# Kernel optimization log

Hardware: AMD Instinct MI355X
Metric: run time of the kernel (lower is better)

The kernel has to match this reference:

```python
import jax, jax.numpy as jnp
import numpy as np

HIDDEN = 4096
NUM_HEADS = 32
NUM_KV_HEADS = 8
HEAD_DIM = 128
ROPE_THETA = 10000.0


def setup_inputs() -> dict:
    key = jax.random.key(0)
    ks = jax.random.split(key, 5)
    B, N = 2, 2048
    s = 0.02
    return {
        "hidden_states": jax.random.normal(ks[0], (B, N, HIDDEN), dtype=jnp.float32),
        "positions": jnp.tile(jnp.arange(N, dtype=jnp.int32)[None, :], (B, 1)),
        "Wq": jax.random.normal(ks[1], (HIDDEN, NUM_HEADS * HEAD_DIM), dtype=jnp.float32) * s,
        "Wk": jax.random.normal(ks[2], (HIDDEN, NUM_KV_HEADS * HEAD_DIM), dtype=jnp.float32) * s,
        "Wv": jax.random.normal(ks[3], (HIDDEN, NUM_KV_HEADS * HEAD_DIM), dtype=jnp.float32) * s,
        "Wo": jax.random.normal(ks[4], (NUM_HEADS * HEAD_DIM, HIDDEN), dtype=jnp.float32) * s,
    }


def _rotate_half(x):
    half = x.shape[-1] // 2
    return jnp.concatenate([-x[..., half:], x[..., :half]], axis=-1)


def reference(hidden_states, positions, Wq, Wk, Wv, Wo):
    B, N, _ = hidden_states.shape
    H, KVH, D = NUM_HEADS, NUM_KV_HEADS, HEAD_DIM
    rep = H // KVH

    # projections
    q = (hidden_states @ Wq).reshape(B, N, H, D).transpose(0, 2, 1, 3)     # [B,H,N,D]
    k = (hidden_states @ Wk).reshape(B, N, KVH, D).transpose(0, 2, 1, 3)   # [B,KVH,N,D]
    v = (hidden_states @ Wv).reshape(B, N, KVH, D).transpose(0, 2, 1, 3)   # [B,KVH,N,D]

    # rotary embedding
    inv_freq = 1.0 / (ROPE_THETA ** (jnp.arange(0, D, 2, dtype=jnp.float32) / D))
    freqs = positions.astype(jnp.float32)[..., None] * inv_freq            # [B,N,D/2]
    emb = jnp.concatenate([freqs, freqs], axis=-1)                          # [B,N,D]
    cos = jnp.cos(emb)[:, None, :, :]                                       # [B,1,N,D]
    sin = jnp.sin(emb)[:, None, :, :]
    q = q * cos + _rotate_half(q) * sin
    k = k * cos + _rotate_half(k) * sin

    # GQA attention without materializing repeated k/v:
    # group q heads by kv head (repeat_interleave => q head h uses kv group h//rep)
    qg = q.reshape(B, KVH, rep, N, D)
    scale = 1.0 / jnp.sqrt(jnp.asarray(D, dtype=q.dtype))
    scores = jnp.einsum('bgrnd,bgmd->bgrnm', qg, k) * scale                 # [B,KVH,rep,N,N]
    causal = jnp.tril(jnp.ones((N, N), dtype=bool))
    scores = jnp.where(causal, scores, jnp.finfo(scores.dtype).min)
    attn = jax.nn.softmax(scores, axis=-1)
    out = jnp.einsum('bgrnm,bgmd->bgrnd', attn, v)                          # [B,KVH,rep,N,D]
    out = out.reshape(B, H, N, D).transpose(0, 2, 1, 3).reshape(B, N, H * D)
    return out @ Wo
```

## Files before the change

kernel.cpp:

```cpp
#include <hip/hip_runtime.h>
#include <hip/hip_bf16.h>

typedef __bf16 bf16_t;
typedef float  f32x4  __attribute__((ext_vector_type(4)));
typedef bf16_t bf16x4 __attribute__((ext_vector_type(4)));
typedef bf16_t bf16x8 __attribute__((ext_vector_type(8)));

#define MFMA16(a, b, c) __builtin_amdgcn_mfma_f32_16x16x32_bf16((a), (b), (c), 0, 0, 0)

#define GLOAD_LDS16(g, l)                                                              \
  __builtin_amdgcn_global_load_lds((const __attribute__((address_space(1))) void*)(g), \
                                   (__attribute__((address_space(3))) void*)(l), 16, 0, 0)

#define BARRIER    __builtin_amdgcn_s_barrier()
#define WAIT_LGKM0 asm volatile("s_waitcnt lgkmcnt(0)" ::: "memory")
#define WAIT_LGKM8 asm volatile("s_waitcnt lgkmcnt(8)" ::: "memory")
#define WAIT_VM3   asm volatile("s_waitcnt vmcnt(3)" ::: "memory")
#define WAIT_VM4   asm volatile("s_waitcnt vmcnt(4)" ::: "memory")
#define WAIT_VM0   asm volatile("s_waitcnt vmcnt(0)" ::: "memory")

__global__ __launch_bounds__(256) void cvt_bf16(const float* __restrict__ in,
                                                bf16_t* __restrict__ out, int n4) {
  int stride = gridDim.x * blockDim.x;
  for (int i = blockIdx.x * blockDim.x + threadIdx.x; i < n4; i += stride) {
    f32x4 v = ((const f32x4*)in)[i];
    bf16x4 o;
#pragma unroll
    for (int j = 0; j < 4; ++j) o[j] = (bf16_t)v[j];
    ((bf16x4*)out)[i] = o;
  }
}

__global__ __launch_bounds__(256) void transpose_cvt(const float* __restrict__ in,
                                                     bf16_t* __restrict__ out,
                                                     int R, int C) {
  __shared__ float t[64][65];
  int tr0 = blockIdx.y * 64, tc0 = blockIdx.x * 64;
  int tx = threadIdx.x & 15, ty = threadIdx.x >> 4;
#pragma unroll
  for (int i = 0; i < 4; ++i) {
    f32x4 v = *(const f32x4*)(in + (size_t)(tr0 + ty + 16 * i) * C + tc0 + tx * 4);
#pragma unroll
    for (int j = 0; j < 4; ++j) t[ty + 16 * i][tx * 4 + j] = v[j];
  }
  __syncthreads();
#pragma unroll
  for (int i = 0; i < 4; ++i) {
    bf16x4 o4;
#pragma unroll
    for (int j = 0; j < 4; ++j) o4[j] = (bf16_t)t[tx * 4 + j][ty + 16 * i];
    *(bf16x4*)(out + (size_t)(tc0 + ty + 16 * i) * R + tr0 + tx * 4) = o4;
  }
}

#define LDB8(bf)                                                                         \
  {                                                                                      \
    const int sb_ = bBase0 + (bf)*16384;                                                 \
    _Pragma("unroll") for (int nf = 0; nf < 4; ++nf) {                                   \
      int row_ = brow0 + nf * 16 + ci;                                                   \
      _Pragma("unroll") for (int ks = 0; ks < 2; ++ks)                                   \
          b[nf][ks] = *(const bf16x8*)&lds[sb_ + row_ * 64 + ((ks * 32 + g * 8) ^ co)];  \
    }                                                                                    \
  }

#define LDA4(bf, q)                                                                      \
  {                                                                                      \
    const int sb_ = aBase0 + (bf)*16384;                                                 \
    _Pragma("unroll") for (int j = 0; j < 2; ++j) {                                      \
      int row_ = ((q)*2 + j) * 16 + ci;                                                  \
      _Pragma("unroll") for (int ks = 0; ks < 2; ++ks)                                   \
          a[j][ks] = *(const bf16x8*)&lds[sb_ + row_ * 64 + ((ks * 32 + g * 8) ^ co)];   \
    }                                                                                    \
  }

#define MMQ(q)                                                                           \
  {                                                                                      \
    __builtin_amdgcn_s_setprio(1);                                                       \
    _Pragma("unroll") for (int j = 0; j < 2; ++j)                                        \
        _Pragma("unroll") for (int nf = 0; nf < 4; ++nf)                                 \
            _Pragma("unroll") for (int ks = 0; ks < 2; ++ks)                             \
                acc[(q)*2 + j][nf] = MFMA16(a[j][ks], b[nf][ks], acc[(q)*2 + j][nf]);    \
    __builtin_amdgcn_s_setprio(0);                                                       \
  }

template <int WRITE_BF16>
__global__ __launch_bounds__(512) void gemm8o(const bf16_t* __restrict__ A,
                                              const bf16_t* __restrict__ Bt,
                                              void* __restrict__ Cv,
                                              int N, int K, int ntn) {
  __shared__ alignas(16) bf16_t lds[65536];
  const int tid = threadIdx.x;
  const int lane = tid & 63, w = tid >> 6;
  const int wr = w >> 2, wc = w & 3;
  const int g = lane >> 4, ci = lane & 15;
  const int cpx = gridDim.x >> 3;
  const int wg = ((int)blockIdx.x & 7) * cpx + ((int)blockIdx.x >> 3);
  const int m0 = (wg / ntn) * 256, n0 = (wg % ntn) * 256;
  const int ksw = ((lane & 7) ^ (lane >> 3)) << 3;
  const int aBase0 = wr * 8192;
  const int bBase0 = 32768 + (wc >> 1) * 8192;
  const int brow0 = (wc & 1) * 64;
  const int co = (ci & 7) << 3;

  const bf16_t* As[2] = {A + (size_t)m0 * K, A + (size_t)(m0 + 128) * K};
  const bf16_t* Bs[2] = {Bt + (size_t)n0 * K, Bt + (size_t)(n0 + 128) * K};

  auto stage = [&](const bf16_t* src, int kk, int ldsbase) {
#pragma unroll
    for (int j = 0; j < 2; ++j)
      GLOAD_LDS16(src + (size_t)(j * 64 + w * 8 + (lane >> 3)) * K + kk + ksw,
                  (char*)&lds[ldsbase + (j * 64 + w * 8) * 64]);
  };

  bf16x8 a[2][2], b[4][2];
  f32x4 acc[8][4];
#pragma unroll
  for (int mf = 0; mf < 8; ++mf)
#pragma unroll
    for (int nf = 0; nf < 4; ++nf) acc[mf][nf] = f32x4{0.f, 0.f, 0.f, 0.f};

  stage(As[0], 0, 0);
  stage(As[1], 0, 8192);
  stage(Bs[0], 0, 32768);
  stage(Bs[1], 0, 40960);
  stage(Bs[0], 64, 49152);
  stage(Bs[1], 64, 57344);
  WAIT_VM4;
  BARRIER;

  const int NT2 = K >> 7;
  for (int i = 0; i < NT2; ++i) {
    const int keb = i << 7;
    const int kA1 = keb + 64;
    int e2 = keb + 128;
    if (e2 > K - 64) e2 = K - 64;
    int o2 = keb + 192;
    if (o2 > K - 64) o2 = K - 64;
    LDA4(0, 0) LDB8(0)
    stage(As[0], kA1, 16384);
    WAIT_LGKM8;
    BARRIER; WAIT_LGKM0;
    MMQ(0)
    BARRIER;
    LDA4(0, 1)
    stage(As[1], kA1, 24576);
    BARRIER; WAIT_LGKM0;
    MMQ(1)
    BARRIER;
    LDA4(0, 2)
    stage(Bs[0], e2, 32768);
    BARRIER; WAIT_LGKM0;
    MMQ(2)
    BARRIER;
    LDA4(0, 3)
    stage(Bs[1], e2, 40960);
    BARRIER; WAIT_LGKM0;
    MMQ(3)
    WAIT_VM4;
    BARRIER;
    LDA4(1, 0) LDB8(1)
    stage(As[0], e2, 0);
    WAIT_LGKM8;
    BARRIER; WAIT_LGKM0;
    MMQ(0)
    BARRIER;
    LDA4(1, 1)
    stage(As[1], e2, 8192);
    BARRIER; WAIT_LGKM0;
    MMQ(1)
    BARRIER;
    LDA4(1, 2)
    stage(Bs[0], o2, 49152);
    BARRIER; WAIT_LGKM0;
    MMQ(2)
    BARRIER;
    LDA4(1, 3)
    stage(Bs[1], o2, 57344);
    BARRIER; WAIT_LGKM0;
    MMQ(3)
    WAIT_VM4;
    BARRIER;
  }
  WAIT_VM0;

#pragma unroll
  for (int mf = 0; mf < 8; ++mf) {
#pragma unroll
    for (int nf = 0; nf < 4; ++nf) {
      int grow = m0 + wr * 128 + mf * 16 + g * 4;
      int gcol = n0 + wc * 64 + nf * 16 + ci;
#pragma unroll
      for (int r = 0; r < 4; ++r) {
        if (WRITE_BF16)
          ((bf16_t*)Cv)[(size_t)(grow + r) * N + gcol] = (bf16_t)acc[mf][nf][r];
        else
          ((float*)Cv)[(size_t)(grow + r) * N + gcol] = acc[mf][nf][r];
      }
    }
  }
}

#define QLDB12(bf)                                                                        \
  {                                                                                       \
    const int sb_ = 32768 + (bf)*12288;                                                   \
    _Pragma("unroll") for (int nf = 0; nf < 6; ++nf) {                                    \
      int row_ = wc * 96 + nf * 16 + ci;                                                  \
      _Pragma("unroll") for (int ks = 0; ks < 2; ++ks)                                    \
          b[nf][ks] = *(const bf16x8*)&lds[sb_ + row_ * 64 + ((ks * 32 + g * 8) ^ co)];   \
    }                                                                                     \
  }

#define QLDA2(bf, q)                                                                      \
  {                                                                                       \
    const int sb_ = (bf)*16384;                                                           \
    const int row_ = wr * 64 + (q)*16 + ci;                                               \
    _Pragma("unroll") for (int ks = 0; ks < 2; ++ks)                                      \
        a[ks] = *(const bf16x8*)&lds[sb_ + row_ * 64 + ((ks * 32 + g * 8) ^ co)];         \
  }

#define QMMQ(q)                                                                           \
  {                                                                                       \
    __builtin_amdgcn_s_setprio(1);                                                        \
    _Pragma("unroll") for (int nf = 0; nf < 6; ++nf)                                      \
        _Pragma("unroll") for (int ks = 0; ks < 2; ++ks)                                  \
            acc[q][nf] = MFMA16(a[ks], b[nf][ks], acc[q][nf]);                            \
    __builtin_amdgcn_s_setprio(0);                                                        \
  }

__global__ __launch_bounds__(512) void gemm8qkv(const bf16_t* __restrict__ A,
                                                const bf16_t* __restrict__ Bt,
                                                bf16_t* __restrict__ C,
                                                int N, int K, int ntn) {
  __shared__ alignas(16) bf16_t lds[57344];
  const int tid = threadIdx.x;
  const int lane = tid & 63, w = tid >> 6;
  const int wr = w >> 1, wc = w & 1;
  const int g = lane >> 4, ci = lane & 15;
  const int cpx = gridDim.x >> 3;
  const int wg = ((int)blockIdx.x & 7) * cpx + ((int)blockIdx.x >> 3);
  const int m0 = (wg / ntn) * 256, n0 = (wg % ntn) * 192;
  const int ksw = ((lane & 7) ^ (lane >> 3)) << 3;
  const int co = (ci & 7) << 3;

  const bf16_t* Ar[4] = {A + (size_t)m0 * K, A + (size_t)(m0 + 64) * K,
                         A + (size_t)(m0 + 128) * K, A + (size_t)(m0 + 192) * K};
  const bf16_t* Br[3] = {Bt + (size_t)n0 * K, Bt + (size_t)(n0 + 64) * K,
                         Bt + (size_t)(n0 + 128) * K};

  auto stage64 = [&](const bf16_t* src, int kk, int ldsbase) {
    GLOAD_LDS16(src + (size_t)(w * 8 + (lane >> 3)) * K + kk + ksw,
                (char*)&lds[ldsbase + w * 512]);
  };

  bf16x8 a[2], b[6][2];
  f32x4 acc[4][6];
#pragma unroll
  for (int mf = 0; mf < 4; ++mf)
#pragma unroll
    for (int nf = 0; nf < 6; ++nf) acc[mf][nf] = f32x4{0.f, 0.f, 0.f, 0.f};

#pragma unroll
  for (int c = 0; c < 4; ++c) stage64(Ar[c], 0, c * 4096);
#pragma unroll
  for (int c = 0; c < 3; ++c) stage64(Br[c], 0, 32768 + c * 4096);
#pragma unroll
  for (int c = 0; c < 3; ++c) stage64(Br[c], 64, 45056 + c * 4096);
  WAIT_VM3;
  BARRIER;

  const int NT2 = K >> 7;
  for (int i = 0; i < NT2; ++i) {
    const int keb = i << 7;
    const int kA1 = keb + 64;
    int e2 = keb + 128;
    if (e2 > K - 64) e2 = K - 64;
    int o2 = keb + 192;
    if (o2 > K - 64) o2 = K - 64;
    QLDA2(0, 0) QLDB12(0)
    stage64(Ar[0], kA1, 16384);
    stage64(Ar[1], kA1, 16384 + 4096);
    WAIT_LGKM8;
    BARRIER; WAIT_LGKM0;
    QMMQ(0)
    BARRIER;
    QLDA2(0, 1)
    stage64(Ar[2], kA1, 16384 + 8192);
    stage64(Ar[3], kA1, 16384 + 12288);
    BARRIER; WAIT_LGKM0;
    QMMQ(1)
    BARRIER;
    QLDA2(0, 2)
    stage64(Br[0], e2, 32768);
    stage64(Br[1], e2, 32768 + 4096);
    BARRIER; WAIT_LGKM0;
    QMMQ(2)
    BARRIER;
    QLDA2(0, 3)
    stage64(Br[2], e2, 32768 + 8192);
    BARRIER; WAIT_LGKM0;
    QMMQ(3)
    WAIT_VM3;
    BARRIER;
    QLDA2(1, 0) QLDB12(1)
    stage64(Ar[0], e2, 0);
    stage64(Ar[1], e2, 4096);
    WAIT_LGKM8;
    BARRIER; WAIT_LGKM0;
    QMMQ(0)
    BARRIER;
    QLDA2(1, 1)
    stage64(Ar[2], e2, 8192);
    stage64(Ar[3], e2, 12288);
    BARRIER; WAIT_LGKM0;
    QMMQ(1)
    BARRIER;
    QLDA2(1, 2)
    stage64(Br[0], o2, 45056);
    stage64(Br[1], o2, 45056 + 4096);
    BARRIER; WAIT_LGKM0;
    QMMQ(2)
    BARRIER;
    QLDA2(1, 3)
    stage64(Br[2], o2, 45056 + 8192);
    BARRIER; WAIT_LGKM0;
    QMMQ(3)
    WAIT_VM3;
    BARRIER;
  }
  WAIT_VM0;

#pragma unroll
  for (int mf = 0; mf < 4; ++mf) {
#pragma unroll
    for (int nf = 0; nf < 6; ++nf) {
      int grow = m0 + wr * 64 + mf * 16 + g * 4;
      int gcol = n0 + wc * 96 + nf * 16 + ci;
#pragma unroll
      for (int r = 0; r < 4; ++r)
        C[(size_t)(grow + r) * N + gcol] = (bf16_t)acc[mf][nf][r];
    }
  }
}

__global__ __launch_bounds__(256) void rope_pack(const bf16_t* __restrict__ QKV,
                                                 const int* __restrict__ pos,
                                                 bf16_t* __restrict__ Qr,
                                                 bf16_t* __restrict__ Kr,
                                                 bf16_t* __restrict__ Vr) {
  int unit = blockIdx.x * 4 + (threadIdx.x >> 6);
  int lane = threadIdx.x & 63;
  int token = unit / 48, slot = unit % 48;
  int b = token >> 11, n = token & 2047;
  const bf16_t* base = QKV + (size_t)token * 6144;
  if (slot < 40) {
    float p = (float)pos[token];
    float inv = exp2f(-(float)lane * 0.20762050593045702f);
    float ang = p * inv;
    float sn, cs;
    sincosf(ang, &sn, &cs);
    const bf16_t* src;
    bf16_t* dst;
    if (slot < 32) {
      src = base + slot * 128;
      dst = Qr + ((size_t)(b * 32 + slot) * 2048 + n) * 128;
    } else {
      int kvh = slot - 32;
      src = base + 4096 + kvh * 128;
      dst = Kr + ((size_t)(b * 8 + kvh) * 2048 + n) * 128;
    }
    float x0 = (float)src[lane], x1 = (float)src[lane + 64];
    dst[lane] = (bf16_t)(x0 * cs - x1 * sn);
    dst[lane + 64] = (bf16_t)(x1 * cs + x0 * sn);
  } else {
    int kvh = slot - 40;
    const bf16_t* src = base + 5120 + kvh * 128;
    bf16_t* dst = Vr + ((size_t)(b * 8 + kvh) * 2048 + n) * 128;
    dst[lane] = src[lane];
    dst[lane + 64] = src[lane + 64];
  }
}

__global__ __launch_bounds__(512) void attn_kernel(const bf16_t* __restrict__ Q,
                                                   const bf16_t* __restrict__ K,
                                                   const bf16_t* __restrict__ V,
                                                   bf16_t* __restrict__ O) {
  const float scale = 0.08838834764831845f;
  __shared__ alignas(16) bf16_t Kl[64 * 128];
  __shared__ alignas(16) bf16_t Vt[128 * 64];
  __shared__ alignas(16) bf16_t Pl[8][32 * 64];
  const int tid = threadIdx.x;
  const int lane = tid & 63, w = tid >> 6;
  const int g = lane >> 4, ci = lane & 15;
  const int hb = blockIdx.y;
  const int b = hb >> 5, h = hb & 31, kvh = h >> 2;
  const int p = blockIdx.x;
  const int qtB = 15 - p;
  const int qr[2] = {p * 128 + w * 16, qtB * 128 + w * 16};
  const bf16_t* Qh = Q + (size_t)hb * 2048 * 128;
  const bf16_t* Kh = K + (size_t)(b * 8 + kvh) * 2048 * 128;
  const bf16_t* Vh = V + (size_t)(b * 8 + kvh) * 2048 * 128;

  bf16x8 bq[2][4];
#pragma unroll
  for (int qb = 0; qb < 2; ++qb)
#pragma unroll
    for (int ks = 0; ks < 4; ++ks)
      bq[qb][ks] = *(const bf16x8*)(Qh + (size_t)(qr[qb] + ci) * 128 + ks * 32 + g * 8);

  f32x4 o[2][8];
#pragma unroll
  for (int qb = 0; qb < 2; ++qb)
#pragma unroll
    for (int nb = 0; nb < 8; ++nb) o[qb][nb] = f32x4{0.f, 0.f, 0.f, 0.f};
  float mrow[2] = {-1e30f, -1e30f};
  float lrow[2] = {0.f, 0.f};

  bf16x8 kreg[2];
  bf16x4 rv[4];
  const int kq = tid >> 5, dq = tid & 31;
  auto loadKV = [&](int kv0) {
#pragma unroll
    for (int i = 0; i < 2; ++i) {
      int c = tid + i * 512;
      kreg[i] = *(const bf16x8*)(Kh + (size_t)(kv0 + (c >> 4)) * 128 + (c & 15) * 8);
    }
#pragma unroll
    for (int rr = 0; rr < 4; ++rr)
      rv[rr] = *(const bf16x4*)(Vh + (size_t)(kv0 + kq * 4 + rr) * 128 + dq * 4);
  };
  auto writeKV = [&]() {
#pragma unroll
    for (int i = 0; i < 2; ++i) {
      int c = tid + i * 512;
      int row = c >> 4, kc = (c & 15) * 8;
      int sw = ((row ^ (row >> 3)) & 7) << 4;
      *(bf16x8*)((char*)Kl + row * 256 + ((kc * 2) ^ sw)) = kreg[i];
    }
#pragma unroll
    for (int jj = 0; jj < 4; ++jj) {
      int d = dq * 4 + jj;
      bf16x4 cv;
#pragma unroll
      for (int rr = 0; rr < 4; ++rr) cv[rr] = rv[rr][jj];
      int sw = ((d ^ (d >> 3)) & 7) << 4;
      *(bf16x4*)((char*)Vt + d * 128 + ((kq * 8) ^ sw)) = cv;
    }
  };

  const int nt = (qtB + 1) * 2;
  loadKV(0);
  for (int t = 0; t < nt; ++t) {
    const int kv0 = t * 64;
    __syncthreads();
    writeKV();
    __syncthreads();
    if (t + 1 < nt) loadKV(kv0 + 64);

    bool act[2] = {kv0 <= qr[0] + 15, kv0 <= qr[1] + 15};
#pragma unroll
    for (int qb = 0; qb < 2; ++qb) {
      if (!act[qb]) continue;
      f32x4 st[4];
#pragma unroll
      for (int kvb = 0; kvb < 4; ++kvb) st[kvb] = f32x4{0.f, 0.f, 0.f, 0.f};
      __builtin_amdgcn_s_setprio(1);
#pragma unroll
      for (int kvb = 0; kvb < 4; ++kvb) {
        int row = kvb * 16 + ci;
        int sw = ((row ^ (row >> 3)) & 7) << 4;
#pragma unroll
        for (int ks = 0; ks < 4; ++ks) {
          bf16x8 ak = *(const bf16x8*)((char*)Kl + row * 256 + ((ks * 64 + g * 16) ^ sw));
          st[kvb] = MFMA16(ak, bq[qb][ks], st[kvb]);
        }
      }
      __builtin_amdgcn_s_setprio(0);
      const int q = qr[qb] + ci;
      const bool needmask = (kv0 + 63 > qr[qb]);
      float pv[16];
      float pm = -1e30f;
#pragma unroll
      for (int kvb = 0; kvb < 4; ++kvb)
#pragma unroll
        for (int r = 0; r < 4; ++r) {
          float v = st[kvb][r] * scale;
          if (needmask && (kv0 + kvb * 16 + 4 * g + r > q)) v = -1e30f;
          pv[kvb * 4 + r] = v;
          pm = fmaxf(pm, v);
        }
      pm = fmaxf(pm, __shfl_xor(pm, 16));
      pm = fmaxf(pm, __shfl_xor(pm, 32));
      const bool nskip = !__all((int)(pm <= mrow[qb] + 8.0f));
      const float mold = mrow[qb];
      float mnew = mold;
      float fs = 1.0f;
      if (nskip) {
        mnew = fmaxf(mold, pm);
        fs = __expf(mold - mnew);
        mrow[qb] = mnew;
      }
      float ps = 0.f;
#pragma unroll
      for (int e = 0; e < 16; ++e) {
        pv[e] = __expf(pv[e] - mnew);
        ps += pv[e];
      }
      ps += __shfl_xor(ps, 16);
      ps += __shfl_xor(ps, 32);
      lrow[qb] = (nskip ? lrow[qb] * fs : lrow[qb]) + ps;
      int prow = qb * 16 + ci;
      int swp = ((prow ^ (prow >> 3)) & 7) << 4;
#pragma unroll
      for (int kvb = 0; kvb < 4; ++kvb) {
        bf16x4 pk;
#pragma unroll
        for (int r = 0; r < 4; ++r) pk[r] = (bf16_t)pv[kvb * 4 + r];
        *(bf16x4*)((char*)&Pl[w][0] + prow * 128 + (((kvb * 16 + 4 * g) * 2) ^ swp)) = pk;
      }
      if (nskip) {
        float fo[4];
#pragma unroll
        for (int r = 0; r < 4; ++r) fo[r] = __shfl(fs, 4 * g + r);
#pragma unroll
        for (int nb = 0; nb < 8; ++nb)
#pragma unroll
          for (int r = 0; r < 4; ++r) o[qb][nb][r] *= fo[r];
      }
    }
    bf16x8 pa[2][2];
#pragma unroll
    for (int qb = 0; qb < 2; ++qb) {
      if (!act[qb]) continue;
      int prow = qb * 16 + ci;
      int swp = ((prow ^ (prow >> 3)) & 7) << 4;
#pragma unroll
      for (int ks = 0; ks < 2; ++ks)
        pa[qb][ks] = *(const bf16x8*)((char*)&Pl[w][0] + prow * 128 + ((ks * 64 + g * 16) ^ swp));
    }
    __builtin_amdgcn_s_setprio(1);
#pragma unroll
    for (int nb = 0; nb < 8; ++nb) {
      int d = nb * 16 + ci;
      int sw = ((d ^ (d >> 3)) & 7) << 4;
      bf16x8 bv0 = *(const bf16x8*)((char*)Vt + d * 128 + ((g * 16) ^ sw));
      bf16x8 bv1 = *(const bf16x8*)((char*)Vt + d * 128 + ((64 + g * 16) ^ sw));
#pragma unroll
      for (int qb = 0; qb < 2; ++qb) {
        if (!act[qb]) continue;
        o[qb][nb] = MFMA16(pa[qb][0], bv0, o[qb][nb]);
        o[qb][nb] = MFMA16(pa[qb][1], bv1, o[qb][nb]);
      }
    }
    __builtin_amdgcn_s_setprio(0);
  }
#pragma unroll
  for (int qb = 0; qb < 2; ++qb) {
    float linv = 1.0f / lrow[qb];
    float lv[4];
#pragma unroll
    for (int r = 0; r < 4; ++r) lv[r] = __shfl(linv, 4 * g + r);
#pragma unroll
    for (int r = 0; r < 4; ++r) {
      int n = qr[qb] + 4 * g + r;
      bf16_t* op = O + (size_t)(b * 2048 + n) * 4096 + h * 128;
#pragma unroll
      for (int nb = 0; nb < 8; ++nb) op[nb * 16 + ci] = (bf16_t)(o[qb][nb][r] * lv[r]);
    }
  }
}

extern "C" void kernel_launch(void* const* d_in, const int* in_sizes, int n_in,
                              void* d_out, int out_size, void* d_ws, size_t ws_size,
                              hipStream_t stream) {
  (void)in_sizes; (void)n_in; (void)out_size; (void)ws_size;
  const float* X = (const float*)d_in[0];
  const int* pos = (const int*)d_in[1];
  const float* Wq = (const float*)d_in[2];
  const float* Wk = (const float*)d_in[3];
  const float* Wv = (const float*)d_in[4];
  const float* Wo = (const float*)d_in[5];
  float* out = (float*)d_out;

  char* w = (char*)d_ws;
  auto carve = [&](size_t bytes) {
    void* p = (void*)w;
    w += (bytes + 255) & ~(size_t)255;
    return p;
  };
  const size_t T = 4096;
  bf16_t* Xbf    = (bf16_t*)carve(T * 4096 * 2);
  bf16_t* WqkvT  = (bf16_t*)carve(6144ull * 4096 * 2);
  bf16_t* WoT    = (bf16_t*)carve(4096ull * 4096 * 2);
  bf16_t* QKVraw = (bf16_t*)carve(T * 6144 * 2);
  bf16_t* Qr     = (bf16_t*)carve(T * 4096 * 2);
  bf16_t* Kr     = (bf16_t*)carve(T * 1024 * 2);
  bf16_t* Vr     = (bf16_t*)carve(T * 1024 * 2);
  bf16_t* Obf    = (bf16_t*)carve(T * 4096 * 2);

  cvt_bf16<<<2048, 256, 0, stream>>>(X, Xbf, (int)(T * 4096 / 4));
  transpose_cvt<<<dim3(64, 64), 256, 0, stream>>>(Wq, WqkvT, 4096, 4096);
  transpose_cvt<<<dim3(16, 64), 256, 0, stream>>>(Wk, WqkvT + 4096ull * 4096, 4096, 1024);
  transpose_cvt<<<dim3(16, 64), 256, 0, stream>>>(Wv, WqkvT + 5120ull * 4096, 4096, 1024);
  transpose_cvt<<<dim3(64, 64), 256, 0, stream>>>(Wo, WoT, 4096, 4096);

  gemm8qkv<<<512, 512, 0, stream>>>(Xbf, WqkvT, QKVraw, 6144, 4096, 32);

  rope_pack<<<(int)(T * 48 / 4), 256, 0, stream>>>(QKVraw, pos, Qr, Kr, Vr);

  attn_kernel<<<dim3(8, 64), 512, 0, stream>>>(Qr, Kr, Vr, Obf);

  gemm8o<0><<<256, 512, 0, stream>>>(Obf, WoT, out, 4096, 4096, 16);
}
```

Measured before the change: 540.4 us.

## Double-buffer K/V tiles in LDS and switch softmax to exp2

```diff
diff --git a/kernel.cpp b/kernel.cpp
--- a/kernel.cpp
+++ b/kernel.cpp
@@ -384,9 +384,9 @@
                                                    const bf16_t* __restrict__ K,
                                                    const bf16_t* __restrict__ V,
                                                    bf16_t* __restrict__ O) {
-  const float scale = 0.08838834764831845f;
-  __shared__ alignas(16) bf16_t Kl[64 * 128];
-  __shared__ alignas(16) bf16_t Vt[128 * 64];
+  const float scale2 = 0.12751743f;
+  __shared__ alignas(16) bf16_t Kl[2 * 64 * 128];
+  __shared__ alignas(16) bf16_t Vt[2 * 128 * 64];
   __shared__ alignas(16) bf16_t Pl[8][32 * 64];
   const int tid = threadIdx.x;
   const int lane = tid & 63, w = tid >> 6;
@@ -428,13 +428,13 @@
     for (int rr = 0; rr < 4; ++rr)
       rv[rr] = *(const bf16x4*)(Vh + (size_t)(kv0 + kq * 4 + rr) * 128 + dq * 4);
   };
-  auto writeKV = [&]() {
+  auto writeKV = [&](int dst) {
 #pragma unroll
     for (int i = 0; i < 2; ++i) {
       int c = tid + i * 512;
       int row = c >> 4, kc = (c & 15) * 8;
       int sw = ((row ^ (row >> 3)) & 7) << 4;
-      *(bf16x8*)((char*)Kl + row * 256 + ((kc * 2) ^ sw)) = kreg[i];
+      *(bf16x8*)((char*)Kl + dst * 16384 + row * 256 + ((kc * 2) ^ sw)) = kreg[i];
     }
 #pragma unroll
     for (int jj = 0; jj < 4; ++jj) {
@@ -443,18 +443,22 @@
 #pragma unroll
       for (int rr = 0; rr < 4; ++rr) cv[rr] = rv[rr][jj];
       int sw = ((d ^ (d >> 3)) & 7) << 4;
-      *(bf16x4*)((char*)Vt + d * 128 + ((kq * 8) ^ sw)) = cv;
+      *(bf16x4*)((char*)Vt + dst * 16384 + d * 128 + ((kq * 8) ^ sw)) = cv;
     }
   };
 
   const int nt = (qtB + 1) * 2;
   loadKV(0);
+  writeKV(0);
+  loadKV(64);
+  WAIT_LGKM0;
+  BARRIER;
+
   for (int t = 0; t < nt; ++t) {
     const int kv0 = t * 64;
-    __syncthreads();
-    writeKV();
-    __syncthreads();
-    if (t + 1 < nt) loadKV(kv0 + 64);
+    const int cur = t & 1;
+    if (t + 1 < nt) writeKV(cur ^ 1);
+    if (t + 2 < nt) loadKV(kv0 + 128);
 
     bool act[2] = {kv0 <= qr[0] + 15, kv0 <= qr[1] + 15};
 #pragma unroll
@@ -470,7 +474,8 @@
         int sw = ((row ^ (row >> 3)) & 7) << 4;
 #pragma unroll
         for (int ks = 0; ks < 4; ++ks) {
-          bf16x8 ak = *(const bf16x8*)((char*)Kl + row * 256 + ((ks * 64 + g * 16) ^ sw));
+          bf16x8 ak = *(const bf16x8*)((char*)Kl + cur * 16384 + row * 256 +
+                                       ((ks * 64 + g * 16) ^ sw));
           st[kvb] = MFMA16(ak, bq[qb][ks], st[kvb]);
         }
       }
@@ -483,26 +488,26 @@
       for (int kvb = 0; kvb < 4; ++kvb)
 #pragma unroll
         for (int r = 0; r < 4; ++r) {
-          float v = st[kvb][r] * scale;
+          float v = st[kvb][r] * scale2;
           if (needmask && (kv0 + kvb * 16 + 4 * g + r > q)) v = -1e30f;
           pv[kvb * 4 + r] = v;
           pm = fmaxf(pm, v);
         }
       pm = fmaxf(pm, __shfl_xor(pm, 16));
       pm = fmaxf(pm, __shfl_xor(pm, 32));
-      const bool nskip = !__all((int)(pm <= mrow[qb] + 8.0f));
+      const bool nskip = !__all((int)(pm <= mrow[qb] + 11.5f));
       const float mold = mrow[qb];
       float mnew = mold;
       float fs = 1.0f;
       if (nskip) {
         mnew = fmaxf(mold, pm);
-        fs = __expf(mold - mnew);
+        fs = exp2f(mold - mnew);
         mrow[qb] = mnew;
       }
       float ps = 0.f;
 #pragma unroll
       for (int e = 0; e < 16; ++e) {
-        pv[e] = __expf(pv[e] - mnew);
+        pv[e] = exp2f(pv[e] - mnew);
         ps += pv[e];
       }
       ps += __shfl_xor(ps, 16);
@@ -542,8 +547,8 @@
     for (int nb = 0; nb < 8; ++nb) {
       int d = nb * 16 + ci;
       int sw = ((d ^ (d >> 3)) & 7) << 4;
-      bf16x8 bv0 = *(const bf16x8*)((char*)Vt + d * 128 + ((g * 16) ^ sw));
-      bf16x8 bv1 = *(const bf16x8*)((char*)Vt + d * 128 + ((64 + g * 16) ^ sw));
+      bf16x8 bv0 = *(const bf16x8*)((char*)Vt + cur * 16384 + d * 128 + ((g * 16) ^ sw));
+      bf16x8 bv1 = *(const bf16x8*)((char*)Vt + cur * 16384 + d * 128 + ((64 + g * 16) ^ sw));
 #pragma unroll
       for (int qb = 0; qb < 2; ++qb) {
         if (!act[qb]) continue;
@@ -552,6 +557,8 @@
       }
     }
     __builtin_amdgcn_s_setprio(0);
+    WAIT_LGKM0;
+    BARRIER;
   }
 #pragma unroll
   for (int qb = 0; qb < 2; ++qb) {
```

New measurement: 612.0 us. 13.2% more time.

## Fuse Q rotary and V read into attention, use exp2 softmax

Applied to the files above, without the earlier changes.

```diff
diff --git a/kernel.cpp b/kernel.cpp
--- a/kernel.cpp
+++ b/kernel.cpp
@@ -3,6 +3,7 @@
 
 typedef __bf16 bf16_t;
 typedef float  f32x4  __attribute__((ext_vector_type(4)));
+typedef bf16_t bf16x2 __attribute__((ext_vector_type(2)));
 typedef bf16_t bf16x4 __attribute__((ext_vector_type(4)));
 typedef bf16_t bf16x8 __attribute__((ext_vector_type(8)));
 
@@ -342,49 +343,37 @@
   }
 }
 
-__global__ __launch_bounds__(256) void rope_pack(const bf16_t* __restrict__ QKV,
-                                                 const int* __restrict__ pos,
-                                                 bf16_t* __restrict__ Qr,
-                                                 bf16_t* __restrict__ Kr,
-                                                 bf16_t* __restrict__ Vr) {
-  int unit = blockIdx.x * 4 + (threadIdx.x >> 6);
-  int lane = threadIdx.x & 63;
-  int token = unit / 48, slot = unit % 48;
+__global__ __launch_bounds__(256) void rope_k(const bf16_t* __restrict__ QKV,
+                                              const int* __restrict__ pos,
+                                              bf16_t* __restrict__ Kr) {
+  int unit = blockIdx.x * 8 + (threadIdx.x >> 5);
+  int l = threadIdx.x & 31;
+  int token = unit >> 3, kvh = unit & 7;
   int b = token >> 11, n = token & 2047;
-  const bf16_t* base = QKV + (size_t)token * 6144;
-  if (slot < 40) {
-    float p = (float)pos[token];
-    float inv = exp2f(-(float)lane * 0.20762050593045702f);
-    float ang = p * inv;
-    float sn, cs;
-    sincosf(ang, &sn, &cs);
-    const bf16_t* src;
-    bf16_t* dst;
-    if (slot < 32) {
-      src = base + slot * 128;
-      dst = Qr + ((size_t)(b * 32 + slot) * 2048 + n) * 128;
-    } else {
-      int kvh = slot - 32;
-      src = base + 4096 + kvh * 128;
-      dst = Kr + ((size_t)(b * 8 + kvh) * 2048 + n) * 128;
-    }
-    float x0 = (float)src[lane], x1 = (float)src[lane + 64];
-    dst[lane] = (bf16_t)(x0 * cs - x1 * sn);
-    dst[lane + 64] = (bf16_t)(x1 * cs + x0 * sn);
-  } else {
-    int kvh = slot - 40;
-    const bf16_t* src = base + 5120 + kvh * 128;
-    bf16_t* dst = Vr + ((size_t)(b * 8 + kvh) * 2048 + n) * 128;
-    dst[lane] = src[lane];
-    dst[lane + 64] = src[lane + 64];
-  }
+  const bf16_t* src = QKV + (size_t)token * 6144 + 4096 + kvh * 128;
+  bf16_t* dst = Kr + ((size_t)(b * 8 + kvh) * 2048 + n) * 128;
+  float p = (float)pos[token];
+  float a0 = p * exp2f(-(float)(2 * l) * 0.20762050593045702f);
+  float a1 = p * exp2f(-(float)(2 * l + 1) * 0.20762050593045702f);
+  float sn0, cs0, sn1, cs1;
+  sincosf(a0, &sn0, &cs0);
+  sincosf(a1, &sn1, &cs1);
+  bf16x2 x0 = *(const bf16x2*)(src + 2 * l);
+  bf16x2 x1 = *(const bf16x2*)(src + 64 + 2 * l);
+  bf16x2 o0, o1;
+  o0[0] = (bf16_t)((float)x0[0] * cs0 - (float)x1[0] * sn0);
+  o0[1] = (bf16_t)((float)x0[1] * cs1 - (float)x1[1] * sn1);
+  o1[0] = (bf16_t)((float)x1[0] * cs0 + (float)x0[0] * sn0);
+  o1[1] = (bf16_t)((float)x1[1] * cs1 + (float)x0[1] * sn1);
+  *(bf16x2*)(dst + 2 * l) = o0;
+  *(bf16x2*)(dst + 64 + 2 * l) = o1;
 }
 
-__global__ __launch_bounds__(512) void attn_kernel(const bf16_t* __restrict__ Q,
+__global__ __launch_bounds__(512) void attn_kernel(const bf16_t* __restrict__ QKV,
                                                    const bf16_t* __restrict__ K,
-                                                   const bf16_t* __restrict__ V,
+                                                   const int* __restrict__ pos,
                                                    bf16_t* __restrict__ O) {
-  const float scale = 0.08838834764831845f;
+  const float scale2 = 0.12751743f;
   __shared__ alignas(16) bf16_t Kl[64 * 128];
   __shared__ alignas(16) bf16_t Vt[128 * 64];
   __shared__ alignas(16) bf16_t Pl[8][32 * 64];
@@ -396,16 +385,30 @@
   const int p = blockIdx.x;
   const int qtB = 15 - p;
   const int qr[2] = {p * 128 + w * 16, qtB * 128 + w * 16};
-  const bf16_t* Qh = Q + (size_t)hb * 2048 * 128;
   const bf16_t* Kh = K + (size_t)(b * 8 + kvh) * 2048 * 128;
-  const bf16_t* Vh = V + (size_t)(b * 8 + kvh) * 2048 * 128;
 
   bf16x8 bq[2][4];
 #pragma unroll
-  for (int qb = 0; qb < 2; ++qb)
-#pragma unroll
-    for (int ks = 0; ks < 4; ++ks)
-      bq[qb][ks] = *(const bf16x8*)(Qh + (size_t)(qr[qb] + ci) * 128 + ks * 32 + g * 8);
+  for (int qb = 0; qb < 2; ++qb) {
+    const int n = qr[qb] + ci;
+    const bf16_t* qp = QKV + (size_t)(b * 2048 + n) * 6144 + h * 128;
+    bf16x8 raw[4];
+#pragma unroll
+    for (int ks = 0; ks < 4; ++ks) raw[ks] = *(const bf16x8*)(qp + ks * 32 + g * 8);
+    float ppos = (float)pos[b * 2048 + n];
+#pragma unroll
+    for (int k2 = 0; k2 < 2; ++k2)
+#pragma unroll
+      for (int j = 0; j < 8; ++j) {
+        int d = k2 * 32 + g * 8 + j;
+        float ang = ppos * exp2f(-(float)d * 0.20762050593045702f);
+        float sn, cs;
+        sincosf(ang, &sn, &cs);
+        float x0 = (float)raw[k2][j], x1 = (float)raw[k2 + 2][j];
+        bq[qb][k2][j] = (bf16_t)(x0 * cs - x1 * sn);
+        bq[qb][k2 + 2][j] = (bf16_t)(x1 * cs + x0 * sn);
+      }
+  }
 
   f32x4 o[2][8];
 #pragma unroll
@@ -426,7 +429,8 @@
     }
 #pragma unroll
     for (int rr = 0; rr < 4; ++rr)
-      rv[rr] = *(const bf16x4*)(Vh + (size_t)(kv0 + kq * 4 + rr) * 128 + dq * 4);
+      rv[rr] = *(const bf16x4*)(QKV + (size_t)(b * 2048 + kv0 + kq * 4 + rr) * 6144 +
+                                5120 + kvh * 128 + dq * 4);
   };
   auto writeKV = [&]() {
 #pragma unroll
@@ -483,26 +487,26 @@
       for (int kvb = 0; kvb < 4; ++kvb)
 #pragma unroll
         for (int r = 0; r < 4; ++r) {
-          float v = st[kvb][r] * scale;
+          float v = st[kvb][r] * scale2;
           if (needmask && (kv0 + kvb * 16 + 4 * g + r > q)) v = -1e30f;
           pv[kvb * 4 + r] = v;
           pm = fmaxf(pm, v);
         }
       pm = fmaxf(pm, __shfl_xor(pm, 16));
       pm = fmaxf(pm, __shfl_xor(pm, 32));
-      const bool nskip = !__all((int)(pm <= mrow[qb] + 8.0f));
+      const bool nskip = !__all((int)(pm <= mrow[qb] + 11.5f));
       const float mold = mrow[qb];
       float mnew = mold;
       float fs = 1.0f;
       if (nskip) {
         mnew = fmaxf(mold, pm);
-        fs = __expf(mold - mnew);
+        fs = exp2f(mold - mnew);
         mrow[qb] = mnew;
       }
       float ps = 0.f;
 #pragma unroll
       for (int e = 0; e < 16; ++e) {
-        pv[e] = __expf(pv[e] - mnew);
+        pv[e] = exp2f(pv[e] - mnew);
         ps += pv[e];
       }
       ps += __shfl_xor(ps, 16);
@@ -592,9 +596,7 @@
   bf16_t* WqkvT  = (bf16_t*)carve(6144ull * 4096 * 2);
   bf16_t* WoT    = (bf16_t*)carve(4096ull * 4096 * 2);
   bf16_t* QKVraw = (bf16_t*)carve(T * 6144 * 2);
-  bf16_t* Qr     = (bf16_t*)carve(T * 4096 * 2);
   bf16_t* Kr     = (bf16_t*)carve(T * 1024 * 2);
-  bf16_t* Vr     = (bf16_t*)carve(T * 1024 * 2);
   bf16_t* Obf    = (bf16_t*)carve(T * 4096 * 2);
 
   cvt_bf16<<<2048, 256, 0, stream>>>(X, Xbf, (int)(T * 4096 / 4));
@@ -605,9 +607,9 @@
 
   gemm8qkv<<<512, 512, 0, stream>>>(Xbf, WqkvT, QKVraw, 6144, 4096, 32);
 
-  rope_pack<<<(int)(T * 48 / 4), 256, 0, stream>>>(QKVraw, pos, Qr, Kr, Vr);
-
-  attn_kernel<<<dim3(8, 64), 512, 0, stream>>>(Qr, Kr, Vr, Obf);
+  rope_k<<<(int)(T * 8 / 8), 256, 0, stream>>>(QKVraw, pos, Kr);
+
+  attn_kernel<<<dim3(8, 64), 512, 0, stream>>>(QKVraw, Kr, pos, Obf);
 
   gemm8o<0><<<256, 512, 0, stream>>>(Obf, WoT, out, 4096, 4096, 16);
 }
```

New measurement: 536.9 us. About the same (-0.7%).
